# Kernel optimization log

Hardware: AMD Instinct MI355X
Metric: run time of the kernel (lower is better)

The kernel has to match this reference:

```python
import jax, jax.numpy as jnp
import numpy as np

N_NODES = 20000
N_EDGES = 640000
B = 256
GNN_DIM = 256
HID = 512
INNER = 2048
RANK = 512
N_CLASSES = 3
N_GENES = 6640


def _ln(x, s, b, eps=1e-5):
    mu = jnp.mean(x, axis=-1, keepdims=True)
    var = jnp.mean(jnp.square(x - mu), axis=-1, keepdims=True)
    return (x - mu) * jax.lax.rsqrt(var + eps) * s + b


def setup_inputs() -> dict:
    key = jax.random.key(0)
    ks = jax.random.split(key, 16)
    s = 0.02
    return {
        "node_indices": jax.random.randint(ks[0], (B,), 0, N_NODES, dtype=jnp.int32),
        "edge_index": jax.random.randint(ks[1], (2, N_EDGES), 0, N_NODES, dtype=jnp.int32),
        "edge_weight": jax.random.uniform(ks[2], (N_EDGES,), dtype=jnp.float32),
        "partial_emb": jax.random.normal(ks[3], (N_NODES, GNN_DIM), dtype=jnp.float32),
        "oov_emb": jnp.zeros((1, GNN_DIM), jnp.float32),
        "gnn_ln_s": jnp.ones((3, GNN_DIM), jnp.float32),
        "gnn_ln_b": jnp.zeros((3, GNN_DIM), jnp.float32),
        "gnn_w": jax.random.normal(ks[4], (3, GNN_DIM, GNN_DIM), jnp.float32) * s,
        "gnn_b": jnp.zeros((3, GNN_DIM), jnp.float32),
        "post_w": jax.random.normal(ks[5], (GNN_DIM, GNN_DIM), jnp.float32) * s,
        "post_b": jnp.zeros((GNN_DIM,), jnp.float32),
        "pin_w": jax.random.normal(ks[6], (GNN_DIM, HID), jnp.float32) * s,
        "pin_b": jnp.zeros((HID,), jnp.float32),
        "blk_ln_s": jnp.ones((6, HID), jnp.float32),
        "blk_ln_b": jnp.zeros((6, HID), jnp.float32),
        "blk_w1": jax.random.normal(ks[7], (6, HID, INNER), jnp.float32) * s,
        "blk_b1": jnp.zeros((6, INNER), jnp.float32),
        "blk_w2": jax.random.normal(ks[8], (6, INNER, HID), jnp.float32) * s,
        "blk_b2": jnp.zeros((6, HID), jnp.float32),
        "pout_w": jax.random.normal(ks[9], (HID, N_CLASSES * RANK), jnp.float32) * s,
        "pout_b": jnp.zeros((N_CLASSES * RANK,), jnp.float32),
        "out_gene_emb": jax.random.normal(ks[10], (N_GENES, RANK), jnp.float32) * s,
    }


def reference(node_indices, edge_index, edge_weight, partial_emb, oov_emb,
              gnn_ln_s, gnn_ln_b, gnn_w, gnn_b, post_w, post_b,
              pin_w, pin_b, blk_ln_s, blk_ln_b, blk_w1, blk_b1, blk_w2, blk_b2,
              pout_w, pout_b, out_gene_emb):
    n = partial_emb.shape[0]
    src, dst = edge_index[0], edge_index[1]
    # --- trainable GNN tail: 3 layers of (LN -> weighted scatter-sum -> Linear -> ReLU) + residual ---
    x = partial_emb
    for i in range(3):
        h = _ln(x, gnn_ln_s[i], gnn_ln_b[i])
        msg = h[src] * edge_weight[:, None]              # [E, 256] gather (memory-bound)
        agg = jax.ops.segment_sum(msg, dst, num_segments=n)
        h = jax.nn.relu(agg @ gnn_w[i] + gnn_b[i])
        x = h + x
    x = x @ post_w + post_b                              # post_mp
    # --- OOV-safe perturbation embedding lookup ---
    oov = node_indices < 0
    safe = jnp.where(oov, 0, node_indices)
    pert = jnp.where(oov[:, None], oov_emb, x[safe])     # [B, 256]
    # --- bilinear head ---
    h = pert @ pin_w + pin_b
    for i in range(6):
        z = _ln(h, blk_ln_s[i], blk_ln_b[i])
        z = jax.nn.gelu(z @ blk_w1[i] + blk_b1[i], approximate=False)
        h = h + z @ blk_w2[i] + blk_b2[i]                # dropout = identity (eval)
    proj = (h @ pout_w + pout_b).reshape(h.shape[0], N_CLASSES, RANK)
    logits = jnp.einsum('bcr,gr->bcg', proj, out_gene_emb)
    return logits
```

## Files before the change

kernel.cpp:

```cpp
#include <hip/hip_runtime.h>
#include <hip/hip_bf16.h>
#include <math.h>

#define NNODES 20000
#define NEDGES 640000
#define BSZ 256
#define GDIM 256
#define HID 512
#define INNER 2048
#define RANK 512
#define NCLS 3
#define NGENES 6640

typedef __attribute__((ext_vector_type(8))) short bf16x8;
typedef __attribute__((ext_vector_type(4))) float f32x4;
typedef __attribute__((ext_vector_type(4))) unsigned u32x4;

__device__ inline float bf2f(unsigned short u) {
    return __uint_as_float(((unsigned)u) << 16);
}
__device__ inline unsigned short f2bf(float f) {
    unsigned u = __float_as_uint(f);
    u = u + 0x7fff + ((u >> 16) & 1);
    return (unsigned short)(u >> 16);
}
__device__ inline unsigned pk2(float a, float b) {
    return (unsigned)f2bf(a) | ((unsigned)f2bf(b) << 16);
}

__device__ inline u32x4 ld16_cg(const void* p) {
    u32x4 r;
    asm volatile("global_load_dwordx4 %0, %1, off sc0 sc1" : "=v"(r) : "v"(p) : "memory");
    return r;
}
__device__ inline void st4f_cg(void* p, float v) {
    asm volatile("global_store_dword %0, %1, off sc0 sc1" :: "v"(p), "v"(v) : "memory");
}
__device__ inline void st2_cg(void* p, unsigned short v) {
    unsigned w = v;
    asm volatile("global_store_short %0, %1, off sc0 sc1" :: "v"(p), "v"(w) : "memory");
}
__device__ inline void waitvm0(void) {
    asm volatile("s_waitcnt vmcnt(0)" ::: "memory");
    __builtin_amdgcn_sched_barrier(0);
}

__global__ void hist_k(const int* __restrict__ dst, int* __restrict__ counts, int E) {
    int e = blockIdx.x * 256 + threadIdx.x;
    if (e < E) atomicAdd(&counts[dst[e]], 1);
}

__global__ void scan1_k(const int* __restrict__ counts, int* __restrict__ incl,
                        int* __restrict__ bsums, int n) {
    __shared__ int s[256];
    int i = blockIdx.x * 256 + threadIdx.x;
    int v = (i < n) ? counts[i] : 0;
    s[threadIdx.x] = v;
    __syncthreads();
    for (int off = 1; off < 256; off <<= 1) {
        int t = (threadIdx.x >= off) ? s[threadIdx.x - off] : 0;
        __syncthreads();
        s[threadIdx.x] += t;
        __syncthreads();
    }
    if (i < n) incl[i] = s[threadIdx.x];
    if (threadIdx.x == 255) bsums[blockIdx.x] = s[255];
}

__global__ void scan2_k(const int* __restrict__ bsums, int* __restrict__ boffs, int nb) {
    __shared__ int s[128];
    int tid = threadIdx.x;
    int v = (tid < nb) ? bsums[tid] : 0;
    s[tid] = v;
    __syncthreads();
    for (int off = 1; off < 128; off <<= 1) {
        int t = (tid >= off) ? s[tid - off] : 0;
        __syncthreads();
        s[tid] += t;
        __syncthreads();
    }
    if (tid < nb) boffs[tid] = s[tid] - v;
}

__global__ void scan3_k(const int* __restrict__ incl, const int* __restrict__ counts,
                        const int* __restrict__ boffs, int* __restrict__ row_start,
                        int* __restrict__ cursor, int n) {
    int i = blockIdx.x * 256 + threadIdx.x;
    if (i < n) {
        int st = incl[i] - counts[i] + boffs[blockIdx.x];
        row_start[i] = st;
        cursor[i] = st;
    }
}

__global__ void scatter_k(const int* __restrict__ src, const int* __restrict__ dst,
                          const float* __restrict__ w, int* __restrict__ cursor,
                          int2* __restrict__ ep, int E) {
    int e = blockIdx.x * 256 + threadIdx.x;
    if (e < E) {
        int d = dst[e];
        int p = atomicAdd(&cursor[d], 1);
        ep[p] = make_int2(src[e], __float_as_int(w[e]));
    }
}

__global__ void flag_k(const int* __restrict__ idx, const int* __restrict__ row_start,
                       const int* __restrict__ counts, const int2* __restrict__ ep,
                       int* __restrict__ flag) {
    int r4 = blockIdx.x * 4 + (threadIdx.x >> 6);
    int lane = threadIdx.x & 63;
    int id = idx[r4];
    int row = id < 0 ? 0 : id;
    if (lane == 0) flag[row] = 1;
    int beg = row_start[row], cnt = counts[row];
    for (int t = lane; t < cnt; t += 64) flag[ep[beg + t].x] = 1;
}

__global__ void convall_k(const float* __restrict__ gnn_w, const float* __restrict__ post_w,
                          const float* __restrict__ pin_w, const float* __restrict__ blk_w1,
                          const float* __restrict__ blk_w2, const float* __restrict__ pout_w,
                          const float* __restrict__ gene, unsigned short* __restrict__ gnnT,
                          unsigned short* __restrict__ postT, unsigned short* __restrict__ pinT,
                          unsigned short* __restrict__ w1T, unsigned short* __restrict__ w2T,
                          unsigned short* __restrict__ poutT,
                          unsigned short* __restrict__ geneb) {
    int b = blockIdx.x;
    if (b >= 13440) {
        int t = b - 13440;
        const float4* xp = (const float4*)gene;
        int i = t * 512 + threadIdx.x * 2;
        float4 a = xp[i], c = xp[i + 1];
        *(ushort4*)(geneb + (size_t)i * 4) =
            make_ushort4(f2bf(a.x), f2bf(a.y), f2bf(a.z), f2bf(a.w));
        *(ushort4*)(geneb + (size_t)i * 4 + 4) =
            make_ushort4(f2bf(c.x), f2bf(c.y), f2bf(c.z), f2bf(c.w));
        return;
    }
    const float* W;
    unsigned short* WT;
    int K, N, tile;
    if (b < 192) {
        int l = b >> 6;
        tile = b & 63;
        W = gnn_w + (size_t)l * GDIM * GDIM;
        WT = gnnT + (size_t)l * GDIM * GDIM;
        K = GDIM; N = GDIM;
    } else if (b < 256) {
        tile = b - 192; W = post_w; WT = postT; K = GDIM; N = GDIM;
    } else if (b < 384) {
        tile = b - 256; W = pin_w; WT = pinT; K = GDIM; N = HID;
    } else if (b < 6528) {
        int t = b - 384;
        int l = t >> 10;
        tile = t & 1023;
        W = blk_w1 + (size_t)l * HID * INNER;
        WT = w1T + (size_t)l * INNER * HID;
        K = HID; N = INNER;
    } else if (b < 12672) {
        int t = b - 6528;
        int l = t >> 10;
        tile = t & 1023;
        W = blk_w2 + (size_t)l * INNER * HID;
        WT = w2T + (size_t)l * HID * INNER;
        K = INNER; N = HID;
    } else {
        tile = b - 12672; W = pout_w; WT = poutT; K = HID; N = NCLS * RANK;
    }
    __shared__ float s[32][33];
    int ntx = N >> 5;
    int k0 = (tile / ntx) << 5;
    int n0 = (tile % ntx) << 5;
    int tx = threadIdx.x & 31, ty = threadIdx.x >> 5;
#pragma unroll
    for (int i = 0; i < 4; i++)
        s[ty + 8 * i][tx] = W[(size_t)(k0 + ty + 8 * i) * N + n0 + tx];
    __syncthreads();
#pragma unroll
    for (int i = 0; i < 4; i++)
        WT[(size_t)(n0 + ty + 8 * i) * K + k0 + tx] = f2bf(s[tx][ty + 8 * i]);
}

template <bool FLAGGED>
__global__ void lnb_k(const float* __restrict__ X, const float* __restrict__ sc,
                      const float* __restrict__ bi, unsigned short* __restrict__ Y, int M,
                      const int* __restrict__ flag) {
    int row = blockIdx.x * 4 + (threadIdx.x >> 6);
    int lane = threadIdx.x & 63;
    if (row >= M) return;
    if (FLAGGED && !flag[row]) return;
    float4 v = ((const float4*)(X + (size_t)row * GDIM))[lane];
    float sum = v.x + v.y + v.z + v.w;
#pragma unroll
    for (int off = 32; off >= 1; off >>= 1) sum += __shfl_xor(sum, off);
    float mu = sum / GDIM;
    float a = v.x - mu, b = v.y - mu, c = v.z - mu, d = v.w - mu;
    float sq = a * a + b * b + c * c + d * d;
#pragma unroll
    for (int off = 32; off >= 1; off >>= 1) sq += __shfl_xor(sq, off);
    float rstd = rsqrtf(sq / GDIM + 1e-5f);
    float4 s4 = ((const float4*)sc)[lane];
    float4 b4 = ((const float4*)bi)[lane];
    *(ushort4*)(Y + (size_t)row * GDIM + lane * 4) =
        make_ushort4(f2bf(a * rstd * s4.x + b4.x), f2bf(b * rstd * s4.y + b4.y),
                     f2bf(c * rstd * s4.z + b4.z), f2bf(d * rstd * s4.w + b4.w));
}

__device__ inline void agg_row(int beg, int cnt, int lane, const int2* __restrict__ ep,
                               const unsigned short* __restrict__ H, float& a0, float& a1,
                               float& a2, float& a3) {
    int t = 0;
    for (; t + 16 <= cnt; t += 16) {
        int2 e[16];
#pragma unroll
        for (int u = 0; u < 16; u++) e[u] = ep[beg + t + u];
        ushort4 v[16];
#pragma unroll
        for (int u = 0; u < 16; u++)
            v[u] = *(const ushort4*)(H + (size_t)e[u].x * GDIM + lane * 4);
#pragma unroll
        for (int u = 0; u < 16; u++) {
            float w = __int_as_float(e[u].y);
            a0 = fmaf(bf2f(v[u].x), w, a0);
            a1 = fmaf(bf2f(v[u].y), w, a1);
            a2 = fmaf(bf2f(v[u].z), w, a2);
            a3 = fmaf(bf2f(v[u].w), w, a3);
        }
    }
    for (; t + 4 <= cnt; t += 4) {
        int2 e[4];
#pragma unroll
        for (int u = 0; u < 4; u++) e[u] = ep[beg + t + u];
        ushort4 v[4];
#pragma unroll
        for (int u = 0; u < 4; u++)
            v[u] = *(const ushort4*)(H + (size_t)e[u].x * GDIM + lane * 4);
#pragma unroll
        for (int u = 0; u < 4; u++) {
            float w = __int_as_float(e[u].y);
            a0 = fmaf(bf2f(v[u].x), w, a0);
            a1 = fmaf(bf2f(v[u].y), w, a1);
            a2 = fmaf(bf2f(v[u].z), w, a2);
            a3 = fmaf(bf2f(v[u].w), w, a3);
        }
    }
    for (; t < cnt; t++) {
        int2 e = ep[beg + t];
        float w = __int_as_float(e.y);
        ushort4 v = *(const ushort4*)(H + (size_t)e.x * GDIM + lane * 4);
        a0 = fmaf(bf2f(v.x), w, a0);
        a1 = fmaf(bf2f(v.y), w, a1);
        a2 = fmaf(bf2f(v.z), w, a2);
        a3 = fmaf(bf2f(v.w), w, a3);
    }
}

template <bool FLAGGED>
__global__ void aggb_k(const int* __restrict__ row_start, const int* __restrict__ counts,
                       const int2* __restrict__ ep, const unsigned short* __restrict__ H,
                       unsigned short* __restrict__ AGG, int n, const int* __restrict__ flag) {
    int row = blockIdx.x * 4 + (threadIdx.x >> 6);
    int lane = threadIdx.x & 63;
    if (row >= n) return;
    if (FLAGGED && !flag[row]) return;
    float a0 = 0.f, a1 = 0.f, a2 = 0.f, a3 = 0.f;
    agg_row(row_start[row], counts[row], lane, ep, H, a0, a1, a2, a3);
    *(ushort4*)(AGG + (size_t)row * GDIM + lane * 4) =
        make_ushort4(f2bf(a0), f2bf(a1), f2bf(a2), f2bf(a3));
}

__global__ void aggsel_k(const int* __restrict__ idx, const int* __restrict__ row_start,
                         const int* __restrict__ counts, const int2* __restrict__ ep,
                         const unsigned short* __restrict__ H, unsigned short* __restrict__ AGG) {
    int b = blockIdx.x * 4 + (threadIdx.x >> 6);
    int lane = threadIdx.x & 63;
    int id = idx[b];
    int row = id < 0 ? 0 : id;
    float a0 = 0.f, a1 = 0.f, a2 = 0.f, a3 = 0.f;
    agg_row(row_start[row], counts[row], lane, ep, H, a0, a1, a2, a3);
    *(ushort4*)(AGG + (size_t)b * GDIM + lane * 4) =
        make_ushort4(f2bf(a0), f2bf(a1), f2bf(a2), f2bf(a3));
}

template <int ACT, bool RES, bool BIAS>
__global__ __launch_bounds__(256) void mgemm_k(const unsigned short* __restrict__ A,
                                               const unsigned short* __restrict__ BT,
                                               const float* __restrict__ bias,
                                               const float* __restrict__ R,
                                               float* __restrict__ C, int M, int N, int K) {
    __shared__ unsigned short As[128 * 32];
    __shared__ unsigned short Bs[128 * 32];
    int m0 = blockIdx.y * 128, n0 = blockIdx.x * 128;
    int tid = threadIdx.x;
    int wave = tid >> 6, lane = tid & 63;
    int wm = (wave >> 1) * 64, wn = (wave & 1) * 64;
    int lrow = lane & 15, lq = lane >> 4;

    f32x4 acc[4][4];
    const f32x4 zz = {0.f, 0.f, 0.f, 0.f};
#pragma unroll
    for (int i = 0; i < 4; i++)
#pragma unroll
        for (int j = 0; j < 4; j++) acc[i][j] = zz;

    int r0 = tid >> 2;
    int q = tid & 3;

    for (int k0 = 0; k0 < K; k0 += 32) {
#pragma unroll
        for (int p = 0; p < 2; p++) {
            int row = r0 + p * 64;
            int gm = m0 + row;
            uint4 va = make_uint4(0, 0, 0, 0);
            if (gm < M) va = *(const uint4*)(A + (size_t)gm * K + k0 + q * 8);
            *(uint4*)&As[row * 32 + q * 8] = va;
            int gn = n0 + row;
            uint4 vb = make_uint4(0, 0, 0, 0);
            if (gn < N) vb = *(const uint4*)(BT + (size_t)gn * K + k0 + q * 8);
            *(uint4*)&Bs[row * 32 + q * 8] = vb;
        }
        __syncthreads();
        bf16x8 af[4], bf[4];
#pragma unroll
        for (int i = 0; i < 4; i++)
            af[i] = *(const bf16x8*)&As[(wm + i * 16 + lrow) * 32 + lq * 8];
#pragma unroll
        for (int j = 0; j < 4; j++)
            bf[j] = *(const bf16x8*)&Bs[(wn + j * 16 + lrow) * 32 + lq * 8];
#pragma unroll
        for (int i = 0; i < 4; i++)
#pragma unroll
            for (int j = 0; j < 4; j++)
                acc[i][j] =
                    __builtin_amdgcn_mfma_f32_16x16x32_bf16(af[i], bf[j], acc[i][j], 0, 0, 0);
        __syncthreads();
    }

#pragma unroll
    for (int i = 0; i < 4; i++) {
#pragma unroll
        for (int j = 0; j < 4; j++) {
            int gn = n0 + wn + j * 16 + lrow;
            if (gn >= N) continue;
            float bv = BIAS ? bias[gn] : 0.f;
#pragma unroll
            for (int r = 0; r < 4; r++) {
                int gm = m0 + wm + i * 16 + lq * 4 + r;
                if (gm >= M) continue;
                float v = acc[i][j][r] + bv;
                if (ACT == 1) v = fmaxf(v, 0.f);
                if (RES) v += R[(size_t)gm * N + gn];
                C[(size_t)gm * N + gn] = v;
            }
        }
    }
}

template <int ACT, int EPI>
__global__ __launch_bounds__(256) void mfull_k(const unsigned short* __restrict__ A,
                                               const unsigned short* __restrict__ BT,
                                               const float* __restrict__ bias,
                                               const int* __restrict__ idx,
                                               const float* __restrict__ aux,
                                               unsigned short* __restrict__ O, int M, int N,
                                               int K) {
    __shared__ unsigned short As[64 * 32];
    __shared__ unsigned short Bs[64 * 32];
    int m0 = blockIdx.y * 64, n0 = blockIdx.x * 64;
    int tid = threadIdx.x;
    int wave = tid >> 6, lane = tid & 63;
    int wm = wave * 16;
    int lrow = lane & 15, lq = lane >> 4;
    f32x4 acc[4];
    const f32x4 zz = {0.f, 0.f, 0.f, 0.f};
#pragma unroll
    for (int j = 0; j < 4; j++) acc[j] = zz;
    int r0 = tid >> 2;
    int q = tid & 3;
    for (int k0 = 0; k0 < K; k0 += 32) {
        *(uint4*)&As[r0 * 32 + q * 8] = *(const uint4*)(A + (size_t)(m0 + r0) * K + k0 + q * 8);
        *(uint4*)&Bs[r0 * 32 + q * 8] = *(const uint4*)(BT + (size_t)(n0 + r0) * K + k0 + q * 8);
        __syncthreads();
        bf16x8 af = *(const bf16x8*)&As[(wm + lrow) * 32 + lq * 8];
#pragma unroll
        for (int j = 0; j < 4; j++) {
            bf16x8 bfr = *(const bf16x8*)&Bs[(j * 16 + lrow) * 32 + lq * 8];
            acc[j] = __builtin_amdgcn_mfma_f32_16x16x32_bf16(af, bfr, acc[j], 0, 0, 0);
        }
        __syncthreads();
    }
#pragma unroll
    for (int j = 0; j < 4; j++) {
        int gn = n0 + j * 16 + lrow;
        float bv = bias[gn];
#pragma unroll
        for (int r = 0; r < 4; r++) {
            int gm = m0 + wm + lq * 4 + r;
            float v = acc[j][r] + bv;
            if (ACT == 1) v = fmaxf(v, 0.f);
            if (ACT == 2) v = 0.5f * v * (1.f + erff(v * 0.70710678118654752f));
            if (EPI == 2) {
                int id = idx[gm];
                int safe = id < 0 ? 0 : id;
                v += aux[(size_t)safe * N + gn];
            }
            if (EPI == 1) {
                if (idx[gm] < 0) v = aux[gn];
            }
            O[(size_t)gm * N + gn] = f2bf(v);
        }
    }
}


#define HGRID 256
#define LDPA 520
#define GBLK 32

__device__ inline void gsync_arrive(int* bar) {
    waitvm0();
    __syncthreads();
    if (threadIdx.x == 0)
        __hip_atomic_fetch_add(bar, 1, __ATOMIC_RELAXED, __HIP_MEMORY_SCOPE_AGENT);
}
__device__ inline void gsync_wait(int* bar, int target) {
    if (threadIdx.x == 0) {
        while (__hip_atomic_load(bar, __ATOMIC_RELAXED, __HIP_MEMORY_SCOPE_AGENT) < target)
            __builtin_amdgcn_s_sleep(2);
    }
    __builtin_amdgcn_s_barrier();
}

template <int ROWS, int KC, bool CG>
__device__ inline void stage_issue(const unsigned short* src, int ld, u32x4* regs) {
    constexpr int NL = ROWS * KC / 8 / 256;
    int tid = threadIdx.x;
#pragma unroll
    for (int it = 0; it < NL; it++) {
        int unit = it * 256 + tid;
        int row = unit / (KC / 8);
        int ucol = unit % (KC / 8);
        const unsigned short* p = src + (size_t)row * ld + ucol * 8;
        if (CG) regs[it] = ld16_cg(p);
        else regs[it] = *(const u32x4*)p;
    }
}
template <int ROWS, int KC>
__device__ inline void stage_write(unsigned short* dst, const u32x4* regs) {
    constexpr int NL = ROWS * KC / 8 / 256;
    int tid = threadIdx.x;
#pragma unroll
    for (int it = 0; it < NL; it++) {
        int unit = it * 256 + tid;
        int row = unit / (KC / 8);
        int ucol = unit % (KC / 8);
        *(u32x4*)&dst[row * LDPA + ucol * 8] = regs[it];
    }
}

template <int KC>
__device__ inline void mma_all(const unsigned short* As, const unsigned short* Bs, f32x4 acc[2]) {
    int tid = threadIdx.x, wave = tid >> 6, lane = tid & 63;
    int wm = (wave >> 1) * 16, wn = (wave & 1) * 32;
    int lrow = lane & 15, lq = lane >> 4;
#pragma unroll
    for (int kk = 0; kk < KC / 32; kk++) {
        bf16x8 af = *(const bf16x8*)&As[(wm + lrow) * LDPA + kk * 32 + lq * 8];
#pragma unroll
        for (int j = 0; j < 2; j++) {
            bf16x8 bfr = *(const bf16x8*)&Bs[(wn + j * 16 + lrow) * LDPA + kk * 32 + lq * 8];
            acc[j] = __builtin_amdgcn_mfma_f32_16x16x32_bf16(af, bfr, acc[j], 0, 0, 0);
        }
    }
}

__global__ __launch_bounds__(256) void head_k(
    const unsigned short* __restrict__ pertbf, const unsigned short* __restrict__ pinT,
    const float* __restrict__ pin_b, const float* __restrict__ blk_ln_s,
    const float* __restrict__ blk_ln_b, const unsigned short* __restrict__ w1T,
    const float* __restrict__ blk_b1, const unsigned short* __restrict__ w2T,
    const float* __restrict__ blk_b2, const unsigned short* __restrict__ poutT,
    const float* __restrict__ pout_b, float* __restrict__ hbuf,
    unsigned short* __restrict__ z1bf, unsigned short* __restrict__ projb,
    int* __restrict__ bar) {
    __shared__ unsigned short As[32 * LDPA];
    __shared__ unsigned short Bs[64 * LDPA];
    int b = blockIdx.x;
    int g = b >> 5;
    int t = b & 31;
    int* gbar = bar + g * 32;
    int m0 = g * 32;
    int tid = threadIdx.x;
    int wave = tid >> 6, lane = tid & 63;
    int wm = (wave >> 1) * 16, wn = (wave & 1) * 32;
    int lrow = lane & 15, lq = lane >> 4;
    int ph = 0;
    f32x4 acc[2];
    const f32x4 zz = {0.f, 0.f, 0.f, 0.f};
    u32x4 pf[16];

    if (t < 8) {
        int n0 = t * 64;
        u32x4 wreg[8], areg[4];
        stage_issue<64, 256, false>(pinT + (size_t)n0 * GDIM, GDIM, wreg);
        stage_issue<32, 256, false>(pertbf + (size_t)m0 * GDIM, GDIM, areg);
        waitvm0();
        stage_write<64, 256>(Bs, wreg);
        stage_write<32, 256>(As, areg);
        __syncthreads();
        acc[0] = zz; acc[1] = zz;
        mma_all<256>(As, Bs, acc);
#pragma unroll
        for (int j = 0; j < 2; j++) {
            int gn = n0 + wn + j * 16 + lrow;
            float bv = pin_b[gn];
#pragma unroll
            for (int r = 0; r < 4; r++) {
                int gm = m0 + wm + lq * 4 + r;
                st4f_cg(hbuf + (size_t)gm * HID + gn, acc[j][r] + bv);
            }
        }
    }
    gsync_arrive(gbar);
    stage_issue<64, 512, false>(w1T + (size_t)t * 64 * HID, HID, pf);
    gsync_wait(gbar, ++ph * GBLK);

    for (int i = 0; i < 6; i++) {
        {
            int n0 = t * 64;
            u32x4 hreg[16];
#pragma unroll
            for (int rr = 0; rr < 8; rr++) {
                const float* p = hbuf + (size_t)(m0 + wave * 8 + rr) * HID + lane * 8;
                hreg[2 * rr] = ld16_cg(p);
                hreg[2 * rr + 1] = ld16_cg(p + 4);
            }
            stage_write<64, 512>(Bs, pf);
            waitvm0();
            const float* ls = blk_ln_s + (size_t)i * HID;
            const float* lb = blk_ln_b + (size_t)i * HID;
            float4 s0 = ((const float4*)ls)[lane * 2], s1 = ((const float4*)ls)[lane * 2 + 1];
            float4 t0 = ((const float4*)lb)[lane * 2], t1 = ((const float4*)lb)[lane * 2 + 1];
#pragma unroll
            for (int rr = 0; rr < 8; rr++) {
                float f0 = __uint_as_float(hreg[2 * rr][0]);
                float f1 = __uint_as_float(hreg[2 * rr][1]);
                float f2 = __uint_as_float(hreg[2 * rr][2]);
                float f3 = __uint_as_float(hreg[2 * rr][3]);
                float f4 = __uint_as_float(hreg[2 * rr + 1][0]);
                float f5 = __uint_as_float(hreg[2 * rr + 1][1]);
                float f6 = __uint_as_float(hreg[2 * rr + 1][2]);
                float f7 = __uint_as_float(hreg[2 * rr + 1][3]);
                float sum = f0 + f1 + f2 + f3 + f4 + f5 + f6 + f7;
#pragma unroll
                for (int off = 32; off >= 1; off >>= 1) sum += __shfl_xor(sum, off);
                float mu = sum * (1.f / HID);
                float d0 = f0 - mu, d1 = f1 - mu, d2 = f2 - mu, d3 = f3 - mu;
                float d4 = f4 - mu, d5 = f5 - mu, d6 = f6 - mu, d7 = f7 - mu;
                float sq = d0 * d0 + d1 * d1 + d2 * d2 + d3 * d3 + d4 * d4 + d5 * d5 +
                           d6 * d6 + d7 * d7;
#pragma unroll
                for (int off = 32; off >= 1; off >>= 1) sq += __shfl_xor(sq, off);
                float rstd = rsqrtf(sq * (1.f / HID) + 1e-5f);
                u32x4 pk;
                pk[0] = pk2(d0 * rstd * s0.x + t0.x, d1 * rstd * s0.y + t0.y);
                pk[1] = pk2(d2 * rstd * s0.z + t0.z, d3 * rstd * s0.w + t0.w);
                pk[2] = pk2(d4 * rstd * s1.x + t1.x, d5 * rstd * s1.y + t1.y);
                pk[3] = pk2(d6 * rstd * s1.z + t1.z, d7 * rstd * s1.w + t1.w);
                *(u32x4*)&As[(wave * 8 + rr) * LDPA + lane * 8] = pk;
            }
            __syncthreads();
            acc[0] = zz; acc[1] = zz;
            mma_all<512>(As, Bs, acc);
#pragma unroll
            for (int j = 0; j < 2; j++) {
                int gn = n0 + wn + j * 16 + lrow;
                float bv = blk_b1[(size_t)i * INNER + gn];
#pragma unroll
                for (int r = 0; r < 4; r++) {
                    int gm = m0 + wm + lq * 4 + r;
                    float v = acc[j][r] + bv;
                    v = 0.5f * v * (1.f + erff(v * 0.70710678118654752f));
                    st2_cg(z1bf + (size_t)gm * INNER + gn, f2bf(v));
                }
            }
        }
        gsync_arrive(gbar);
        stage_issue<64, 512, false>(
            w2T + (size_t)i * HID * INNER + (size_t)(t & 7) * 64 * INNER + (t >> 3) * 512,
            INNER, pf);
        gsync_wait(gbar, ++ph * GBLK);
        {
            int s = t >> 3, n0 = (t & 7) * 64, kbeg = s * 512;
            u32x4 areg[8];
            stage_issue<32, 512, true>(z1bf + (size_t)m0 * INNER + kbeg, INNER, areg);
            stage_write<64, 512>(Bs, pf);
            waitvm0();
            stage_write<32, 512>(As, areg);
            __syncthreads();
            acc[0] = zz; acc[1] = zz;
            mma_all<512>(As, Bs, acc);
#pragma unroll
            for (int j = 0; j < 2; j++) {
                int gn = n0 + wn + j * 16 + lrow;
                float bv = (s == 0) ? blk_b2[(size_t)i * HID + gn] : 0.f;
#pragma unroll
                for (int r = 0; r < 4; r++) {
                    int gm = m0 + wm + lq * 4 + r;
                    __hip_atomic_fetch_add(hbuf + (size_t)gm * HID + gn, acc[j][r] + bv,
                                           __ATOMIC_RELAXED, __HIP_MEMORY_SCOPE_AGENT);
                }
            }
        }
        gsync_arrive(gbar);
        if (i < 5)
            stage_issue<64, 512, false>(
                w1T + (size_t)(i + 1) * INNER * HID + (size_t)t * 64 * HID, HID, pf);
        else if (t < 24)
            stage_issue<64, 512, false>(poutT + (size_t)t * 64 * HID, HID, pf);
        gsync_wait(gbar, ++ph * GBLK);
    }

    if (t < 24) {
        int n0 = t * 64;
        u32x4 areg[16];
#pragma unroll
        for (int it = 0; it < 16; it++) {
            int unit = it * 256 + tid;
            int row = unit >> 7, ucol = unit & 127;
            areg[it] = ld16_cg(hbuf + (size_t)(m0 + row) * HID + ucol * 4);
        }
        stage_write<64, 512>(Bs, pf);
        waitvm0();
#pragma unroll
        for (int it = 0; it < 16; it++) {
            int unit = it * 256 + tid;
            int row = unit >> 7, ucol = unit & 127;
            float a = __uint_as_float(areg[it][0]), c = __uint_as_float(areg[it][1]);
            float d = __uint_as_float(areg[it][2]), e = __uint_as_float(areg[it][3]);
            uint2 w2v;
            w2v.x = pk2(a, c);
            w2v.y = pk2(d, e);
            *(uint2*)&As[row * LDPA + ucol * 4] = w2v;
        }
        __syncthreads();
        acc[0] = zz; acc[1] = zz;
        mma_all<512>(As, Bs, acc);
#pragma unroll
        for (int j = 0; j < 2; j++) {
            int gn = n0 + wn + j * 16 + lrow;
            float bv = pout_b[gn];
#pragma unroll
            for (int r = 0; r < 4; r++) {
                int gm = m0 + wm + lq * 4 + r;
                projb[(size_t)gm * (NCLS * RANK) + gn] = f2bf(acc[j][r] + bv);
            }
        }
    }
}

extern "C" void kernel_launch(void* const* d_in, const int* in_sizes, int n_in,
                              void* d_out, int out_size, void* d_ws, size_t ws_size,
                              hipStream_t stream) {
    const int* node_indices = (const int*)d_in[0];
    const int* edge_src = (const int*)d_in[1];
    const int* edge_dst = edge_src + NEDGES;
    const float* edge_w = (const float*)d_in[2];
    const float* partial_emb = (const float*)d_in[3];
    const float* oov_emb = (const float*)d_in[4];
    const float* gnn_ln_s = (const float*)d_in[5];
    const float* gnn_ln_b = (const float*)d_in[6];
    const float* gnn_w = (const float*)d_in[7];
    const float* gnn_b = (const float*)d_in[8];
    const float* post_w = (const float*)d_in[9];
    const float* post_b = (const float*)d_in[10];
    const float* pin_w = (const float*)d_in[11];
    const float* pin_b = (const float*)d_in[12];
    const float* blk_ln_s = (const float*)d_in[13];
    const float* blk_ln_b = (const float*)d_in[14];
    const float* blk_w1 = (const float*)d_in[15];
    const float* blk_b1 = (const float*)d_in[16];
    const float* blk_w2 = (const float*)d_in[17];
    const float* blk_b2 = (const float*)d_in[18];
    const float* pout_w = (const float*)d_in[19];
    const float* pout_b = (const float*)d_in[20];
    const float* gene = (const float*)d_in[21];
    float* out = (float*)d_out;

    char* p = (char*)d_ws;
    auto alloc = [&](size_t bytes) {
        char* r = p;
        p += (bytes + 255) & ~(size_t)255;
        return r;
    };
    int* counts = (int*)alloc(NNODES * 4);
    int* incl = (int*)alloc(NNODES * 4);
    int* bsums = (int*)alloc(128 * 4);
    int* boffs = (int*)alloc(128 * 4);
    int* row_start = (int*)alloc(NNODES * 4);
    int* cursor = (int*)alloc(NNODES * 4);
    int* flag = (int*)alloc(NNODES * 4);
    int2* epack = (int2*)alloc((size_t)NEDGES * 8);
    float* part = (float*)alloc((size_t)NNODES * GDIM * 4);
    unsigned short* ln_bf = (unsigned short*)part;
    unsigned short* aggbf = (unsigned short*)((char*)part + (size_t)NNODES * GDIM * 2);
    float* xa = (float*)alloc((size_t)NNODES * GDIM * 4);
    float* xb = (float*)alloc((size_t)NNODES * GDIM * 4);
    float* hbuf = (float*)alloc((size_t)BSZ * HID * 4);
    unsigned short* aggselb = (unsigned short*)alloc((size_t)BSZ * GDIM * 2);
    unsigned short* pertinbf = (unsigned short*)alloc((size_t)BSZ * GDIM * 2);
    unsigned short* pertbf = (unsigned short*)alloc((size_t)BSZ * GDIM * 2);
    unsigned short* z1bf = (unsigned short*)alloc((size_t)BSZ * INNER * 2);
    unsigned short* projb = (unsigned short*)alloc((size_t)BSZ * NCLS * RANK * 2);
    unsigned short* gnnT = (unsigned short*)alloc((size_t)3 * GDIM * GDIM * 2);
    unsigned short* postT = (unsigned short*)alloc((size_t)GDIM * GDIM * 2);
    unsigned short* pinT = (unsigned short*)alloc((size_t)HID * GDIM * 2);
    unsigned short* w1T = (unsigned short*)alloc((size_t)6 * INNER * HID * 2);
    unsigned short* w2T = (unsigned short*)alloc((size_t)6 * HID * INNER * 2);
    unsigned short* poutT = (unsigned short*)alloc((size_t)NCLS * RANK * HID * 2);
    unsigned short* geneb = (unsigned short*)alloc((size_t)NGENES * RANK * 2);
    int* bar = (int*)alloc(1024);

    const int EB = (NEDGES + 255) / 256;
    const int NB = (NNODES + 255) / 256;

    convall_k<<<15100, 256, 0, stream>>>(gnn_w, post_w, pin_w, blk_w1, blk_w2, pout_w, gene,
                                         gnnT, postT, pinT, w1T, w2T, poutT, geneb);

    (void)hipMemsetAsync(counts, 0, NNODES * 4, stream);
    (void)hipMemsetAsync(flag, 0, NNODES * 4, stream);
    (void)hipMemsetAsync(bar, 0, 1024, stream);
    hist_k<<<EB, 256, 0, stream>>>(edge_dst, counts, NEDGES);
    scan1_k<<<NB, 256, 0, stream>>>(counts, incl, bsums, NNODES);
    scan2_k<<<1, 128, 0, stream>>>(bsums, boffs, NB);
    scan3_k<<<NB, 256, 0, stream>>>(incl, counts, boffs, row_start, cursor, NNODES);
    scatter_k<<<EB, 256, 0, stream>>>(edge_src, edge_dst, edge_w, cursor, epack, NEDGES);
    flag_k<<<BSZ / 4, 256, 0, stream>>>(node_indices, row_start, counts, epack, flag);

    const float* x_in = partial_emb;
    float* bufs[2] = {xa, xb};
    for (int i = 0; i < 2; i++) {
        lnb_k<false><<<(NNODES + 3) / 4, 256, 0, stream>>>(
            x_in, gnn_ln_s + i * GDIM, gnn_ln_b + i * GDIM, ln_bf, NNODES, nullptr);
        if (i == 0)
            aggb_k<false><<<(NNODES + 3) / 4, 256, 0, stream>>>(row_start, counts, epack, ln_bf,
                                                                aggbf, NNODES, nullptr);
        else
            aggb_k<true><<<(NNODES + 3) / 4, 256, 0, stream>>>(row_start, counts, epack, ln_bf,
                                                               aggbf, NNODES, flag);
        float* x_out = bufs[i];
        mgemm_k<1, true, true><<<dim3(GDIM / 128, (NNODES + 127) / 128), 256, 0, stream>>>(
            aggbf, gnnT + (size_t)i * GDIM * GDIM, gnn_b + i * GDIM, x_in, x_out, NNODES, GDIM,
            GDIM);
        x_in = x_out;
    }
    lnb_k<true><<<(NNODES + 3) / 4, 256, 0, stream>>>(xb, gnn_ln_s + 2 * GDIM,
                                                      gnn_ln_b + 2 * GDIM, ln_bf, NNODES, flag);
    aggsel_k<<<BSZ / 4, 256, 0, stream>>>(node_indices, row_start, counts, epack, ln_bf, aggselb);
    mfull_k<1, 2><<<dim3(GDIM / 64, BSZ / 64), 256, 0, stream>>>(
        aggselb, gnnT + (size_t)2 * GDIM * GDIM, gnn_b + 2 * GDIM, node_indices, xb, pertinbf,
        BSZ, GDIM, GDIM);

    mfull_k<0, 1><<<dim3(GDIM / 64, BSZ / 64), 256, 0, stream>>>(
        pertinbf, postT, post_b, node_indices, oov_emb, pertbf, BSZ, GDIM, GDIM);

    head_k<<<HGRID, 256, 0, stream>>>(pertbf, pinT, pin_b, blk_ln_s, blk_ln_b, w1T, blk_b1, w2T,
                                      blk_b2, poutT, pout_b, hbuf, z1bf, projb, bar);

    mgemm_k<0, false, false><<<dim3((NGENES + 127) / 128, (BSZ * NCLS) / 128), 256, 0, stream>>>(
        projb, geneb, nullptr, nullptr, out, BSZ * NCLS, NGENES, RANK);
}
```

Before: 514.8 us.

## Fuse selected-row aggregation, last GNN linear and post_mp into persistent head kernel

Moves the last-layer aggregation for the 256 selected nodes, the third GNN linear with ReLU and residual, and the post_mp linear with the OOV substitution into the persistent head kernel. They run as extra phases separated by group-local barriers, replacing three separate kernel launches. Each 32-block group aggregates its own 32 rows, with one row per block and a 4-wave reduction in shared memory. This removes launch overhead and inter-kernel gaps. In exchange it adds three group-barrier phases, and only 4 of 32 blocks per group do the small GEMMs.

Measured after the change: 510.8 us. Within noise of the previous version (-0.8%).

```diff
diff --git a/kernel.cpp b/kernel.cpp
--- a/kernel.cpp
+++ b/kernel.cpp
@@ -15,6 +15,7 @@
 typedef __attribute__((ext_vector_type(8))) short bf16x8;
 typedef __attribute__((ext_vector_type(4))) float f32x4;
 typedef __attribute__((ext_vector_type(4))) unsigned u32x4;
+typedef __attribute__((ext_vector_type(2))) unsigned u32x2;
 
 __device__ inline float bf2f(unsigned short u) {
     return __uint_as_float(((unsigned)u) << 16);
@@ -33,8 +34,16 @@
     asm volatile("global_load_dwordx4 %0, %1, off sc0 sc1" : "=v"(r) : "v"(p) : "memory");
     return r;
 }
+__device__ inline u32x2 ld8_cg(const void* p) {
+    u32x2 r;
+    asm volatile("global_load_dwordx2 %0, %1, off sc0 sc1" : "=v"(r) : "v"(p) : "memory");
+    return r;
+}
 __device__ inline void st4f_cg(void* p, float v) {
     asm volatile("global_store_dword %0, %1, off sc0 sc1" :: "v"(p), "v"(v) : "memory");
+}
+__device__ inline void st8_cg(void* p, u32x2 v) {
+    asm volatile("global_store_dwordx2 %0, %1, off sc0 sc1" :: "v"(p), "v"(v) : "memory");
 }
 __device__ inline void st2_cg(void* p, unsigned short v) {
     unsigned w = v;
@@ -43,6 +52,24 @@
 __device__ inline void waitvm0(void) {
     asm volatile("s_waitcnt vmcnt(0)" ::: "memory");
     __builtin_amdgcn_sched_barrier(0);
+}
+
+__device__ inline void gsync_arrive(int* bar) {
+    waitvm0();
+    __syncthreads();
+    if (threadIdx.x == 0)
+        __hip_atomic_fetch_add(bar, 1, __ATOMIC_RELAXED, __HIP_MEMORY_SCOPE_AGENT);
+}
+__device__ inline void gsync_wait(int* bar, int target) {
+    if (threadIdx.x == 0) {
+        while (__hip_atomic_load(bar, __ATOMIC_RELAXED, __HIP_MEMORY_SCOPE_AGENT) < target)
+            __builtin_amdgcn_s_sleep(2);
+    }
+    __builtin_amdgcn_s_barrier();
+}
+__device__ inline void gsync_c(int* bar, int target) {
+    gsync_arrive(bar);
+    gsync_wait(bar, target);
 }
 
 __global__ void hist_k(const int* __restrict__ dst, int* __restrict__ counts, int E) {
@@ -268,19 +295,6 @@
         make_ushort4(f2bf(a0), f2bf(a1), f2bf(a2), f2bf(a3));
 }
 
-__global__ void aggsel_k(const int* __restrict__ idx, const int* __restrict__ row_start,
-                         const int* __restrict__ counts, const int2* __restrict__ ep,
-                         const unsigned short* __restrict__ H, unsigned short* __restrict__ AGG) {
-    int b = blockIdx.x * 4 + (threadIdx.x >> 6);
-    int lane = threadIdx.x & 63;
-    int id = idx[b];
-    int row = id < 0 ? 0 : id;
-    float a0 = 0.f, a1 = 0.f, a2 = 0.f, a3 = 0.f;
-    agg_row(row_start[row], counts[row], lane, ep, H, a0, a1, a2, a3);
-    *(ushort4*)(AGG + (size_t)b * GDIM + lane * 4) =
-        make_ushort4(f2bf(a0), f2bf(a1), f2bf(a2), f2bf(a3));
-}
-
 template <int ACT, bool RES, bool BIAS>
 __global__ __launch_bounds__(256) void mgemm_k(const unsigned short* __restrict__ A,
                                                const unsigned short* __restrict__ BT,
@@ -355,80 +369,10 @@
     }
 }
 
-template <int ACT, int EPI>
-__global__ __launch_bounds__(256) void mfull_k(const unsigned short* __restrict__ A,
-                                               const unsigned short* __restrict__ BT,
-                                               const float* __restrict__ bias,
-                                               const int* __restrict__ idx,
-                                               const float* __restrict__ aux,
-                                               unsigned short* __restrict__ O, int M, int N,
-                                               int K) {
-    __shared__ unsigned short As[64 * 32];
-    __shared__ unsigned short Bs[64 * 32];
-    int m0 = blockIdx.y * 64, n0 = blockIdx.x * 64;
-    int tid = threadIdx.x;
-    int wave = tid >> 6, lane = tid & 63;
-    int wm = wave * 16;
-    int lrow = lane & 15, lq = lane >> 4;
-    f32x4 acc[4];
-    const f32x4 zz = {0.f, 0.f, 0.f, 0.f};
-#pragma unroll
-    for (int j = 0; j < 4; j++) acc[j] = zz;
-    int r0 = tid >> 2;
-    int q = tid & 3;
-    for (int k0 = 0; k0 < K; k0 += 32) {
-        *(uint4*)&As[r0 * 32 + q * 8] = *(const uint4*)(A + (size_t)(m0 + r0) * K + k0 + q * 8);
-        *(uint4*)&Bs[r0 * 32 + q * 8] = *(const uint4*)(BT + (size_t)(n0 + r0) * K + k0 + q * 8);
-        __syncthreads();
-        bf16x8 af = *(const bf16x8*)&As[(wm + lrow) * 32 + lq * 8];
-#pragma unroll
-        for (int j = 0; j < 4; j++) {
-            bf16x8 bfr = *(const bf16x8*)&Bs[(j * 16 + lrow) * 32 + lq * 8];
-            acc[j] = __builtin_amdgcn_mfma_f32_16x16x32_bf16(af, bfr, acc[j], 0, 0, 0);
-        }
-        __syncthreads();
-    }
-#pragma unroll
-    for (int j = 0; j < 4; j++) {
-        int gn = n0 + j * 16 + lrow;
-        float bv = bias[gn];
-#pragma unroll
-        for (int r = 0; r < 4; r++) {
-            int gm = m0 + wm + lq * 4 + r;
-            float v = acc[j][r] + bv;
-            if (ACT == 1) v = fmaxf(v, 0.f);
-            if (ACT == 2) v = 0.5f * v * (1.f + erff(v * 0.70710678118654752f));
-            if (EPI == 2) {
-                int id = idx[gm];
-                int safe = id < 0 ? 0 : id;
-                v += aux[(size_t)safe * N + gn];
-            }
-            if (EPI == 1) {
-                if (idx[gm] < 0) v = aux[gn];
-            }
-            O[(size_t)gm * N + gn] = f2bf(v);
-        }
-    }
-}
-
 
 #define HGRID 256
 #define LDPA 520
 #define GBLK 32
-
-__device__ inline void gsync_arrive(int* bar) {
-    waitvm0();
-    __syncthreads();
-    if (threadIdx.x == 0)
-        __hip_atomic_fetch_add(bar, 1, __ATOMIC_RELAXED, __HIP_MEMORY_SCOPE_AGENT);
-}
-__device__ inline void gsync_wait(int* bar, int target) {
-    if (threadIdx.x == 0) {
-        while (__hip_atomic_load(bar, __ATOMIC_RELAXED, __HIP_MEMORY_SCOPE_AGENT) < target)
-            __builtin_amdgcn_s_sleep(2);
-    }
-    __builtin_amdgcn_s_barrier();
-}
 
 template <int ROWS, int KC, bool CG>
 __device__ inline void stage_issue(const unsigned short* src, int ld, u32x4* regs) {
@@ -474,14 +418,20 @@
 }
 
 __global__ __launch_bounds__(256) void head_k(
-    const unsigned short* __restrict__ pertbf, const unsigned short* __restrict__ pinT,
-    const float* __restrict__ pin_b, const float* __restrict__ blk_ln_s,
-    const float* __restrict__ blk_ln_b, const unsigned short* __restrict__ w1T,
-    const float* __restrict__ blk_b1, const unsigned short* __restrict__ w2T,
-    const float* __restrict__ blk_b2, const unsigned short* __restrict__ poutT,
-    const float* __restrict__ pout_b, float* __restrict__ hbuf,
-    unsigned short* __restrict__ z1bf, unsigned short* __restrict__ projb,
-    int* __restrict__ bar) {
+    const int* __restrict__ node_indices, const int* __restrict__ row_start,
+    const int* __restrict__ counts, const int2* __restrict__ ep,
+    const unsigned short* __restrict__ lnbf, const unsigned short* __restrict__ gnnT3,
+    const float* __restrict__ gnnb3, const float* __restrict__ xb,
+    const unsigned short* __restrict__ postT, const float* __restrict__ post_b,
+    const float* __restrict__ oov_emb, unsigned short* __restrict__ aggselb,
+    unsigned short* __restrict__ pertinbf, unsigned short* __restrict__ pertbf,
+    const unsigned short* __restrict__ pinT, const float* __restrict__ pin_b,
+    const float* __restrict__ blk_ln_s, const float* __restrict__ blk_ln_b,
+    const unsigned short* __restrict__ w1T, const float* __restrict__ blk_b1,
+    const unsigned short* __restrict__ w2T, const float* __restrict__ blk_b2,
+    const unsigned short* __restrict__ poutT, const float* __restrict__ pout_b,
+    float* __restrict__ hbuf, unsigned short* __restrict__ z1bf,
+    unsigned short* __restrict__ projb, int* __restrict__ bar) {
     __shared__ unsigned short As[32 * LDPA];
     __shared__ unsigned short Bs[64 * LDPA];
     int b = blockIdx.x;
@@ -498,11 +448,103 @@
     const f32x4 zz = {0.f, 0.f, 0.f, 0.f};
     u32x4 pf[16];
 
+    {
+        int bb = m0 + t;
+        int id = node_indices[bb];
+        int row = id < 0 ? 0 : id;
+        int beg = row_start[row], cnt = counts[row];
+        float a0 = 0.f, a1 = 0.f, a2 = 0.f, a3 = 0.f;
+        for (int e2 = wave; e2 < cnt; e2 += 4) {
+            int2 ed = ep[beg + e2];
+            float w = __int_as_float(ed.y);
+            ushort4 v = *(const ushort4*)(lnbf + (size_t)ed.x * GDIM + lane * 4);
+            a0 = fmaf(bf2f(v.x), w, a0);
+            a1 = fmaf(bf2f(v.y), w, a1);
+            a2 = fmaf(bf2f(v.z), w, a2);
+            a3 = fmaf(bf2f(v.w), w, a3);
+        }
+        float* red = (float*)As;
+        red[wave * 256 + lane * 4 + 0] = a0;
+        red[wave * 256 + lane * 4 + 1] = a1;
+        red[wave * 256 + lane * 4 + 2] = a2;
+        red[wave * 256 + lane * 4 + 3] = a3;
+        __syncthreads();
+        if (wave == 0) {
+            float s0 = red[lane * 4] + red[256 + lane * 4] + red[512 + lane * 4] +
+                       red[768 + lane * 4];
+            float s1 = red[lane * 4 + 1] + red[256 + lane * 4 + 1] + red[512 + lane * 4 + 1] +
+                       red[768 + lane * 4 + 1];
+            float s2 = red[lane * 4 + 2] + red[256 + lane * 4 + 2] + red[512 + lane * 4 + 2] +
+                       red[768 + lane * 4 + 2];
+            float s3 = red[lane * 4 + 3] + red[256 + lane * 4 + 3] + red[512 + lane * 4 + 3] +
+                       red[768 + lane * 4 + 3];
+            u32x2 pk;
+            pk[0] = pk2(s0, s1);
+            pk[1] = pk2(s2, s3);
+            st8_cg(aggselb + (size_t)bb * GDIM + lane * 4, pk);
+        }
+    }
+    gsync_c(gbar, ++ph * GBLK);
+
+    if (t < 4) {
+        int n0 = t * 64;
+        u32x4 wreg[8], areg[4];
+        stage_issue<64, 256, false>(gnnT3 + (size_t)n0 * GDIM, GDIM, wreg);
+        stage_issue<32, 256, true>(aggselb + (size_t)m0 * GDIM, GDIM, areg);
+        waitvm0();
+        stage_write<64, 256>(Bs, wreg);
+        stage_write<32, 256>(As, areg);
+        __syncthreads();
+        acc[0] = zz; acc[1] = zz;
+        mma_all<256>(As, Bs, acc);
+#pragma unroll
+        for (int j = 0; j < 2; j++) {
+            int gn = n0 + wn + j * 16 + lrow;
+            float bv = gnnb3[gn];
+#pragma unroll
+            for (int r = 0; r < 4; r++) {
+                int gmb = m0 + wm + lq * 4 + r;
+                float v = fmaxf(acc[j][r] + bv, 0.f);
+                int id = node_indices[gmb];
+                int safe = id < 0 ? 0 : id;
+                v += xb[(size_t)safe * GDIM + gn];
+                st2_cg(pertinbf + (size_t)gmb * GDIM + gn, f2bf(v));
+            }
+        }
+    }
+    gsync_c(gbar, ++ph * GBLK);
+
+    if (t < 4) {
+        int n0 = t * 64;
+        u32x4 wreg[8], areg[4];
+        stage_issue<64, 256, false>(postT + (size_t)n0 * GDIM, GDIM, wreg);
+        stage_issue<32, 256, true>(pertinbf + (size_t)m0 * GDIM, GDIM, areg);
+        waitvm0();
+        stage_write<64, 256>(Bs, wreg);
+        stage_write<32, 256>(As, areg);
+        __syncthreads();
+        acc[0] = zz; acc[1] = zz;
+        mma_all<256>(As, Bs, acc);
+#pragma unroll
+        for (int j = 0; j < 2; j++) {
+            int gn = n0 + wn + j * 16 + lrow;
+            float bv = post_b[gn];
+#pragma unroll
+            for (int r = 0; r < 4; r++) {
+                int gmb = m0 + wm + lq * 4 + r;
+                float v = acc[j][r] + bv;
+                if (node_indices[gmb] < 0) v = oov_emb[gn];
+                st2_cg(pertbf + (size_t)gmb * GDIM + gn, f2bf(v));
+            }
+        }
+    }
+    gsync_c(gbar, ++ph * GBLK);
+
     if (t < 8) {
         int n0 = t * 64;
         u32x4 wreg[8], areg[4];
         stage_issue<64, 256, false>(pinT + (size_t)n0 * GDIM, GDIM, wreg);
-        stage_issue<32, 256, false>(pertbf + (size_t)m0 * GDIM, GDIM, areg);
+        stage_issue<32, 256, true>(pertbf + (size_t)m0 * GDIM, GDIM, areg);
         waitvm0();
         stage_write<64, 256>(Bs, wreg);
         stage_write<32, 256>(As, areg);
@@ -755,16 +797,12 @@
     }
     lnb_k<true><<<(NNODES + 3) / 4, 256, 0, stream>>>(xb, gnn_ln_s + 2 * GDIM,
                                                       gnn_ln_b + 2 * GDIM, ln_bf, NNODES, flag);
-    aggsel_k<<<BSZ / 4, 256, 0, stream>>>(node_indices, row_start, counts, epack, ln_bf, aggselb);
-    mfull_k<1, 2><<<dim3(GDIM / 64, BSZ / 64), 256, 0, stream>>>(
-        aggselb, gnnT + (size_t)2 * GDIM * GDIM, gnn_b + 2 * GDIM, node_indices, xb, pertinbf,
-        BSZ, GDIM, GDIM);
-
-    mfull_k<0, 1><<<dim3(GDIM / 64, BSZ / 64), 256, 0, stream>>>(
-        pertinbf, postT, post_b, node_indices, oov_emb, pertbf, BSZ, GDIM, GDIM);
-
-    head_k<<<HGRID, 256, 0, stream>>>(pertbf, pinT, pin_b, blk_ln_s, blk_ln_b, w1T, blk_b1, w2T,
-                                      blk_b2, poutT, pout_b, hbuf, z1bf, projb, bar);
+
+    head_k<<<HGRID, 256, 0, stream>>>(node_indices, row_start, counts, epack, ln_bf,
+                                      gnnT + (size_t)2 * GDIM * GDIM, gnn_b + 2 * GDIM, xb,
+                                      postT, post_b, oov_emb, aggselb, pertinbf, pertbf, pinT,
+                                      pin_b, blk_ln_s, blk_ln_b, w1T, blk_b1, w2T, blk_b2,
+                                      poutT, pout_b, hbuf, z1bf, projb, bar);
 
     mgemm_k<0, false, false><<<dim3((NGENES + 127) / 128, (BSZ * NCLS) / 128), 256, 0, stream>>>(
         projb, geneb, nullptr, nullptr, out, BSZ * NCLS, NGENES, RANK);
```
